# Optimization experiments

Measured on AMD Instinct MI355X. Metric: run time of the kernel, lower is better.

The kernel has to match this reference:

```python
import jax, jax.numpy as jnp
import numpy as np

E, FX, FE, H, OUT = 1_000_000, 32, 32, 64, 32
LN_EPS = 1e-5


def _ln(x, g, b):
    # LayerNorm over the channel (last) dim, elementwise_affine=True
    m = jnp.mean(x, axis=-1, keepdims=True)
    v = jnp.mean((x - m) ** 2, axis=-1, keepdims=True)
    return (x - m) * jax.lax.rsqrt(v + LN_EPS) * g + b


def setup_inputs() -> dict:
    key = jax.random.key(0)
    ks = jax.random.split(key, 6)
    d0 = 2 * FX + FE  # 96, the concat(src, dest, edge_attr) width
    src = jax.random.normal(ks[0], (E, FX), jnp.float32)
    dest = jax.random.normal(ks[1], (E, FX), jnp.float32)
    edge_attr = jax.random.normal(ks[2], (E, FE), jnp.float32)
    W1 = jax.random.normal(ks[3], (d0, H), jnp.float32) / np.float32(np.sqrt(d0))
    b1 = jnp.zeros((H,), jnp.float32)
    g1 = jnp.ones((H,), jnp.float32)
    be1 = jnp.zeros((H,), jnp.float32)
    W2 = jax.random.normal(ks[4], (H + d0, H), jnp.float32) / np.float32(np.sqrt(H + d0))
    b2 = jnp.zeros((H,), jnp.float32)
    g2 = jnp.ones((H,), jnp.float32)
    be2 = jnp.zeros((H,), jnp.float32)
    W3 = jax.random.normal(ks[5], (H, OUT), jnp.float32) / np.float32(np.sqrt(H))
    b3 = jnp.zeros((OUT,), jnp.float32)
    eb = jnp.zeros((E,), jnp.int32)  # edge-batch ids; unused (no GraphNorm in setup)
    return {"src": src, "dest": dest, "edge_attr": edge_attr,
            "W1": W1, "b1": b1, "g1": g1, "be1": be1,
            "W2": W2, "b2": b2, "g2": g2, "be2": be2,
            "W3": W3, "b3": b3, "eb": eb}


def reference(src, dest, edge_attr, W1, b1, g1, be1, W2, b2, g2, be2, W3, b3, eb):
    # out[0] = cat([src, dest, edge_attr], 1)
    x0 = jnp.concatenate([src, dest, edge_attr], axis=1)            # [E, 96]
    h = _ln(jax.nn.relu(x0 @ W1 + b1), g1, be1)                      # layers 0-2 -> [E, 64]
    # layer 3: shelf [3, 0] -> cat(out[3], out[0])
    h = _ln(jax.nn.relu(jnp.concatenate([h, x0], axis=1) @ W2 + b2), g2, be2)  # layers 3-5
    return h @ W3 + b3                                               # layer 6 -> [E, 32]
```

## Files before the change

### kernel.cpp

```cpp
#include <hip/hip_runtime.h>

typedef __bf16 bf16x8 __attribute__((ext_vector_type(8)));
typedef __bf16 bf16x4 __attribute__((ext_vector_type(4)));
typedef float  f32x4  __attribute__((ext_vector_type(4)));

#define NW 8
#define HPAD 68
#define NFRAG 36
#define LDS_WAIT() asm volatile("s_waitcnt lgkmcnt(0)" ::: "memory")

static __device__ __forceinline__ bf16x8 ld_frag_lds8(const __bf16* p) {
    bf16x4 lo = *(const bf16x4*)p;
    bf16x4 hi = *(const bf16x4*)(p + 4);
    bf16x8 r;
    r[0] = lo[0]; r[1] = lo[1]; r[2] = lo[2]; r[3] = lo[3];
    r[4] = hi[0]; r[5] = hi[1]; r[6] = hi[2]; r[7] = hi[3];
    return r;
}

static __device__ __forceinline__ bf16x8 cvt_frag(float4 v0, float4 v1) {
    bf16x8 r;
    r[0] = (__bf16)v0.x; r[1] = (__bf16)v0.y; r[2] = (__bf16)v0.z; r[3] = (__bf16)v0.w;
    r[4] = (__bf16)v1.x; r[5] = (__bf16)v1.y; r[6] = (__bf16)v1.z; r[7] = (__bf16)v1.w;
    return r;
}

static __device__ __forceinline__ void ln_epilogue(const f32x4* acc, const float* bv,
                                                   const float* gv, const float* ev,
                                                   __bf16* hp, int n16, int q) {
    float u[4][4];
    float sm[4] = {0.f, 0.f, 0.f, 0.f};
    float sq[4] = {0.f, 0.f, 0.f, 0.f};
#pragma unroll
    for (int t = 0; t < 4; ++t)
#pragma unroll
        for (int j = 0; j < 4; ++j) {
            float x = acc[t][j] + bv[t];
            x = fmaxf(x, 0.0f);
            u[t][j] = x;
            sm[j] += x;
            sq[j] += x * x;
        }
#pragma unroll
    for (int msk = 1; msk <= 8; msk <<= 1)
#pragma unroll
        for (int j = 0; j < 4; ++j) {
            sm[j] += __shfl_xor(sm[j], msk, 64);
            sq[j] += __shfl_xor(sq[j], msk, 64);
        }
    float mean[4], rstd[4];
#pragma unroll
    for (int j = 0; j < 4; ++j) {
        mean[j] = sm[j] * 0.015625f;
        float v = sq[j] * 0.015625f - mean[j] * mean[j];
        rstd[j] = rsqrtf(fmaxf(v, 0.0f) + 1e-5f);
    }
#pragma unroll
    for (int t = 0; t < 4; ++t)
#pragma unroll
        for (int j = 0; j < 4; ++j) {
            float y = (u[t][j] - mean[j]) * rstd[j] * gv[t] + ev[t];
            hp[(q * 4 + j) * HPAD + t * 16 + n16] = (__bf16)y;
        }
}

__global__ __launch_bounds__(512, 4)
void edge_model_kernel(const float* __restrict__ srcp,
                       const float* __restrict__ dstp,
                       const float* __restrict__ eap,
                       const float* __restrict__ W1, const float* __restrict__ b1,
                       const float* __restrict__ g1, const float* __restrict__ be1,
                       const float* __restrict__ W2, const float* __restrict__ b2,
                       const float* __restrict__ g2, const float* __restrict__ be2,
                       const float* __restrict__ W3, const float* __restrict__ b3,
                       float* __restrict__ out, int E) {
    __shared__ alignas(16) __bf16 wlds[NFRAG * 64 * 8];
    __shared__ alignas(16) __bf16 hs[NW][2][16 * HPAD];

    const int tid = threadIdx.x;
    const int w   = tid >> 6;
    const int l   = tid & 63;
    const int n16 = l & 15;
    const int q   = l >> 4;

    for (int idx = tid; idx < NFRAG * 64; idx += blockDim.x) {
        int fid = idx >> 6, fl = idx & 63;
        int lq = fl >> 4, ln = fl & 15;
        const float* Wsrc; int ldw, row0, col;
        if (fid < 12)      { int s = fid >> 2,        t = fid & 3;        Wsrc = W1; ldw = 64; row0 = s * 32 + lq * 8; col = t * 16 + ln; }
        else if (fid < 32) { int f = fid - 12, s = f >> 2, t = f & 3;     Wsrc = W2; ldw = 64; row0 = s * 32 + lq * 8; col = t * 16 + ln; }
        else               { int f = fid - 32, s = f >> 1, t = f & 1;     Wsrc = W3; ldw = 32; row0 = s * 32 + lq * 8; col = t * 16 + ln; }
        __bf16* dst = wlds + idx * 8;
#pragma unroll
        for (int jj = 0; jj < 8; ++jj)
            dst[jj] = (__bf16)Wsrc[(row0 + jj) * ldw + col];
    }

    float b1v[4], g1v[4], e1v[4], b2v[4], g2v[4], e2v[4], b3v[2];
#pragma unroll
    for (int t = 0; t < 4; ++t) {
        int c = t * 16 + n16;
        b1v[t] = b1[c]; g1v[t] = g1[c]; e1v[t] = be1[c];
        b2v[t] = b2[c]; g2v[t] = g2[c]; e2v[t] = be2[c];
    }
    b3v[0] = b3[n16];
    b3v[1] = b3[16 + n16];

    __syncthreads();

    const int nTiles = (E + 15) >> 4;
    const int stride = gridDim.x * NW;
    __bf16* h1p = &hs[w][0][0];
    __bf16* h2p = &hs[w][1][0];
    const __bf16* wl = wlds + l * 8;

    int tile = blockIdx.x * NW + w;
    if (tile >= nTiles) return;

    bf16x8 a0[3];
    {
        const size_t abase = (size_t)min((tile << 4) + n16, E - 1) * 32 + q * 8;
        a0[0] = cvt_frag(((const float4*)(srcp + abase))[0], ((const float4*)(srcp + abase))[1]);
        a0[1] = cvt_frag(((const float4*)(dstp + abase))[0], ((const float4*)(dstp + abase))[1]);
        a0[2] = cvt_frag(((const float4*)(eap  + abase))[0], ((const float4*)(eap  + abase))[1]);
    }

    for (;;) {
        const int e0 = tile << 4;
        const int nt = tile + stride;

        const int pt = (nt < nTiles) ? nt : tile;
        const size_t pbase = (size_t)min((pt << 4) + n16, E - 1) * 32 + q * 8;
        float4 p0a = ((const float4*)(srcp + pbase))[0];
        float4 p0b = ((const float4*)(srcp + pbase))[1];
        float4 p1a = ((const float4*)(dstp + pbase))[0];
        float4 p1b = ((const float4*)(dstp + pbase))[1];
        float4 p2a = ((const float4*)(eap  + pbase))[0];
        float4 p2b = ((const float4*)(eap  + pbase))[1];

        f32x4 acc1[4] = {};
#pragma unroll
        for (int s = 0; s < 3; ++s)
#pragma unroll
            for (int t = 0; t < 4; ++t) {
                bf16x8 wf = *(const bf16x8*)(wl + (s * 4 + t) * 512);
                acc1[t] = __builtin_amdgcn_mfma_f32_16x16x32_bf16(a0[s], wf, acc1[t], 0, 0, 0);
            }

        ln_epilogue(acc1, b1v, g1v, e1v, h1p, n16, q);
        LDS_WAIT();

        f32x4 acc2[4] = {};
        bf16x8 h1f0 = ld_frag_lds8(h1p + n16 * HPAD + q * 8);
        bf16x8 h1f1 = ld_frag_lds8(h1p + n16 * HPAD + 32 + q * 8);
#pragma unroll
        for (int t = 0; t < 4; ++t) {
            bf16x8 wf = *(const bf16x8*)(wl + (12 + t) * 512);
            acc2[t] = __builtin_amdgcn_mfma_f32_16x16x32_bf16(h1f0, wf, acc2[t], 0, 0, 0);
        }
#pragma unroll
        for (int t = 0; t < 4; ++t) {
            bf16x8 wf = *(const bf16x8*)(wl + (16 + t) * 512);
            acc2[t] = __builtin_amdgcn_mfma_f32_16x16x32_bf16(h1f1, wf, acc2[t], 0, 0, 0);
        }
#pragma unroll
        for (int s = 0; s < 3; ++s)
#pragma unroll
            for (int t = 0; t < 4; ++t) {
                bf16x8 wf = *(const bf16x8*)(wl + (20 + s * 4 + t) * 512);
                acc2[t] = __builtin_amdgcn_mfma_f32_16x16x32_bf16(a0[s], wf, acc2[t], 0, 0, 0);
            }

        ln_epilogue(acc2, b2v, g2v, e2v, h2p, n16, q);
        LDS_WAIT();

        f32x4 acc3[2] = {};
#pragma unroll
        for (int s = 0; s < 2; ++s) {
            bf16x8 h2f = ld_frag_lds8(h2p + n16 * HPAD + s * 32 + q * 8);
#pragma unroll
            for (int t = 0; t < 2; ++t) {
                bf16x8 wf = *(const bf16x8*)(wl + (32 + s * 2 + t) * 512);
                acc3[t] = __builtin_amdgcn_mfma_f32_16x16x32_bf16(h2f, wf, acc3[t], 0, 0, 0);
            }
        }

#pragma unroll
        for (int t = 0; t < 2; ++t)
#pragma unroll
            for (int j = 0; j < 4; ++j) {
                int r = e0 + q * 4 + j;
                if (r < E) out[(size_t)r * 32 + t * 16 + n16] = acc3[t][j] + b3v[t];
            }

        if (nt >= nTiles) break;
        tile = nt;
        a0[0] = cvt_frag(p0a, p0b);
        a0[1] = cvt_frag(p1a, p1b);
        a0[2] = cvt_frag(p2a, p2b);
    }
}

extern "C" void kernel_launch(void* const* d_in, const int* in_sizes, int n_in,
                              void* d_out, int out_size, void* d_ws, size_t ws_size,
                              hipStream_t stream) {
    (void)n_in; (void)out_size; (void)d_ws; (void)ws_size;
    const float* srcp = (const float*)d_in[0];
    const float* dstp = (const float*)d_in[1];
    const float* eap  = (const float*)d_in[2];
    const float* W1   = (const float*)d_in[3];
    const float* b1   = (const float*)d_in[4];
    const float* g1   = (const float*)d_in[5];
    const float* be1  = (const float*)d_in[6];
    const float* W2   = (const float*)d_in[7];
    const float* b2   = (const float*)d_in[8];
    const float* g2   = (const float*)d_in[9];
    const float* be2  = (const float*)d_in[10];
    const float* W3   = (const float*)d_in[11];
    const float* b3   = (const float*)d_in[12];
    float* out = (float*)d_out;

    const int E = in_sizes[0] / 32;
    const int nTiles = (E + 15) / 16;
    int blocks = (nTiles + NW - 1) / NW;
    if (blocks > 512) blocks = 512;

    edge_model_kernel<<<blocks, 512, 0, stream>>>(srcp, dstp, eap, W1, b1, g1, be1,
                                                  W2, b2, g2, be2, W3, b3, out, E);
}
```

Measured before the change: 414.5 us.

## Process two 16-edge tiles per wave to reuse weight fragments

Each wave now handles a 32-edge super-tile as two independent 16-row MFMA streams that share every weight fragment loaded from LDS. This halves LDS weight reads per edge and interleaves two independent MFMA chains to hide latency. The prefetch of the next super-tile's inputs is moved later, after the second LayerNorm, so fewer registers are live during the first two layers. The cost is doubled accumulator and input-fragment registers, which may spill under launch_bounds(512,4), and fewer waves in flight per edge.

```diff
diff --git a/kernel.cpp b/kernel.cpp
--- a/kernel.cpp
+++ b/kernel.cpp
@@ -108,80 +108,95 @@
 
     __syncthreads();
 
-    const int nTiles = (E + 15) >> 4;
+    const int nSuper = (E + 31) >> 5;
     const int stride = gridDim.x * NW;
-    __bf16* h1p = &hs[w][0][0];
-    __bf16* h2p = &hs[w][1][0];
+    __bf16* hA = &hs[w][0][0];
+    __bf16* hB = &hs[w][1][0];
     const __bf16* wl = wlds + l * 8;
 
-    int tile = blockIdx.x * NW + w;
-    if (tile >= nTiles) return;
-
-    bf16x8 a0[3];
+    int st = blockIdx.x * NW + w;
+    if (st >= nSuper) return;
+
+    bf16x8 a0A[3], a0B[3];
     {
-        const size_t abase = (size_t)min((tile << 4) + n16, E - 1) * 32 + q * 8;
-        a0[0] = cvt_frag(((const float4*)(srcp + abase))[0], ((const float4*)(srcp + abase))[1]);
-        a0[1] = cvt_frag(((const float4*)(dstp + abase))[0], ((const float4*)(dstp + abase))[1]);
-        a0[2] = cvt_frag(((const float4*)(eap  + abase))[0], ((const float4*)(eap  + abase))[1]);
+        const size_t baA = (size_t)min((st << 5) + n16,      E - 1) * 32 + q * 8;
+        const size_t baB = (size_t)min((st << 5) + 16 + n16, E - 1) * 32 + q * 8;
+        a0A[0] = cvt_frag(((const float4*)(srcp + baA))[0], ((const float4*)(srcp + baA))[1]);
+        a0A[1] = cvt_frag(((const float4*)(dstp + baA))[0], ((const float4*)(dstp + baA))[1]);
+        a0A[2] = cvt_frag(((const float4*)(eap  + baA))[0], ((const float4*)(eap  + baA))[1]);
+        a0B[0] = cvt_frag(((const float4*)(srcp + baB))[0], ((const float4*)(srcp + baB))[1]);
+        a0B[1] = cvt_frag(((const float4*)(dstp + baB))[0], ((const float4*)(dstp + baB))[1]);
+        a0B[2] = cvt_frag(((const float4*)(eap  + baB))[0], ((const float4*)(eap  + baB))[1]);
     }
 
     for (;;) {
-        const int e0 = tile << 4;
-        const int nt = tile + stride;
-
-        const int pt = (nt < nTiles) ? nt : tile;
-        const size_t pbase = (size_t)min((pt << 4) + n16, E - 1) * 32 + q * 8;
-        float4 p0a = ((const float4*)(srcp + pbase))[0];
-        float4 p0b = ((const float4*)(srcp + pbase))[1];
-        float4 p1a = ((const float4*)(dstp + pbase))[0];
-        float4 p1b = ((const float4*)(dstp + pbase))[1];
-        float4 p2a = ((const float4*)(eap  + pbase))[0];
-        float4 p2b = ((const float4*)(eap  + pbase))[1];
-
-        f32x4 acc1[4] = {};
+        const int e0 = st << 5;
+        const int ns = st + stride;
+
+        f32x4 accA1[4] = {}, accB1[4] = {};
 #pragma unroll
         for (int s = 0; s < 3; ++s)
 #pragma unroll
             for (int t = 0; t < 4; ++t) {
                 bf16x8 wf = *(const bf16x8*)(wl + (s * 4 + t) * 512);
-                acc1[t] = __builtin_amdgcn_mfma_f32_16x16x32_bf16(a0[s], wf, acc1[t], 0, 0, 0);
-            }
-
-        ln_epilogue(acc1, b1v, g1v, e1v, h1p, n16, q);
+                accA1[t] = __builtin_amdgcn_mfma_f32_16x16x32_bf16(a0A[s], wf, accA1[t], 0, 0, 0);
+                accB1[t] = __builtin_amdgcn_mfma_f32_16x16x32_bf16(a0B[s], wf, accB1[t], 0, 0, 0);
+            }
+
+        ln_epilogue(accA1, b1v, g1v, e1v, hA, n16, q);
+        ln_epilogue(accB1, b1v, g1v, e1v, hB, n16, q);
         LDS_WAIT();
 
-        f32x4 acc2[4] = {};
-        bf16x8 h1f0 = ld_frag_lds8(h1p + n16 * HPAD + q * 8);
-        bf16x8 h1f1 = ld_frag_lds8(h1p + n16 * HPAD + 32 + q * 8);
+        f32x4 accA2[4] = {}, accB2[4] = {};
+        bf16x8 hA0 = ld_frag_lds8(hA + n16 * HPAD + q * 8);
+        bf16x8 hA1 = ld_frag_lds8(hA + n16 * HPAD + 32 + q * 8);
+        bf16x8 hB0 = ld_frag_lds8(hB + n16 * HPAD + q * 8);
+        bf16x8 hB1 = ld_frag_lds8(hB + n16 * HPAD + 32 + q * 8);
 #pragma unroll
         for (int t = 0; t < 4; ++t) {
             bf16x8 wf = *(const bf16x8*)(wl + (12 + t) * 512);
-            acc2[t] = __builtin_amdgcn_mfma_f32_16x16x32_bf16(h1f0, wf, acc2[t], 0, 0, 0);
+            accA2[t] = __builtin_amdgcn_mfma_f32_16x16x32_bf16(hA0, wf, accA2[t], 0, 0, 0);
+            accB2[t] = __builtin_amdgcn_mfma_f32_16x16x32_bf16(hB0, wf, accB2[t], 0, 0, 0);
         }
 #pragma unroll
         for (int t = 0; t < 4; ++t) {
             bf16x8 wf = *(const bf16x8*)(wl + (16 + t) * 512);
-            acc2[t] = __builtin_amdgcn_mfma_f32_16x16x32_bf16(h1f1, wf, acc2[t], 0, 0, 0);
+            accA2[t] = __builtin_amdgcn_mfma_f32_16x16x32_bf16(hA1, wf, accA2[t], 0, 0, 0);
+            accB2[t] = __builtin_amdgcn_mfma_f32_16x16x32_bf16(hB1, wf, accB2[t], 0, 0, 0);
         }
 #pragma unroll
         for (int s = 0; s < 3; ++s)
 #pragma unroll
             for (int t = 0; t < 4; ++t) {
                 bf16x8 wf = *(const bf16x8*)(wl + (20 + s * 4 + t) * 512);
-                acc2[t] = __builtin_amdgcn_mfma_f32_16x16x32_bf16(a0[s], wf, acc2[t], 0, 0, 0);
-            }
-
-        ln_epilogue(acc2, b2v, g2v, e2v, h2p, n16, q);
+                accA2[t] = __builtin_amdgcn_mfma_f32_16x16x32_bf16(a0A[s], wf, accA2[t], 0, 0, 0);
+                accB2[t] = __builtin_amdgcn_mfma_f32_16x16x32_bf16(a0B[s], wf, accB2[t], 0, 0, 0);
+            }
+
+        ln_epilogue(accA2, b2v, g2v, e2v, hA, n16, q);
+        ln_epilogue(accB2, b2v, g2v, e2v, hB, n16, q);
         LDS_WAIT();
 
-        f32x4 acc3[2] = {};
+        const int pt = (ns < nSuper) ? ns : st;
+        const size_t pbA = (size_t)min((pt << 5) + n16,      E - 1) * 32 + q * 8;
+        const size_t pbB = (size_t)min((pt << 5) + 16 + n16, E - 1) * 32 + q * 8;
+        float4 pA0a = ((const float4*)(srcp + pbA))[0], pA0b = ((const float4*)(srcp + pbA))[1];
+        float4 pA1a = ((const float4*)(dstp + pbA))[0], pA1b = ((const float4*)(dstp + pbA))[1];
+        float4 pA2a = ((const float4*)(eap  + pbA))[0], pA2b = ((const float4*)(eap  + pbA))[1];
+        float4 pB0a = ((const float4*)(srcp + pbB))[0], pB0b = ((const float4*)(srcp + pbB))[1];
+        float4 pB1a = ((const float4*)(dstp + pbB))[0], pB1b = ((const float4*)(dstp + pbB))[1];
+        float4 pB2a = ((const float4*)(eap  + pbB))[0], pB2b = ((const float4*)(eap  + pbB))[1];
+
+        f32x4 accA3[2] = {}, accB3[2] = {};
 #pragma unroll
         for (int s = 0; s < 2; ++s) {
-            bf16x8 h2f = ld_frag_lds8(h2p + n16 * HPAD + s * 32 + q * 8);
+            bf16x8 hfA = ld_frag_lds8(hA + n16 * HPAD + s * 32 + q * 8);
+            bf16x8 hfB = ld_frag_lds8(hB + n16 * HPAD + s * 32 + q * 8);
 #pragma unroll
             for (int t = 0; t < 2; ++t) {
                 bf16x8 wf = *(const bf16x8*)(wl + (32 + s * 2 + t) * 512);
-                acc3[t] = __builtin_amdgcn_mfma_f32_16x16x32_bf16(h2f, wf, acc3[t], 0, 0, 0);
+                accA3[t] = __builtin_amdgcn_mfma_f32_16x16x32_bf16(hfA, wf, accA3[t], 0, 0, 0);
+                accB3[t] = __builtin_amdgcn_mfma_f32_16x16x32_bf16(hfB, wf, accB3[t], 0, 0, 0);
             }
         }
 
@@ -189,15 +204,20 @@
         for (int t = 0; t < 2; ++t)
 #pragma unroll
             for (int j = 0; j < 4; ++j) {
-                int r = e0 + q * 4 + j;
-                if (r < E) out[(size_t)r * 32 + t * 16 + n16] = acc3[t][j] + b3v[t];
-            }
-
-        if (nt >= nTiles) break;
-        tile = nt;
-        a0[0] = cvt_frag(p0a, p0b);
-        a0[1] = cvt_frag(p1a, p1b);
-        a0[2] = cvt_frag(p2a, p2b);
+                int rA = e0 + q * 4 + j;
+                int rB = e0 + 16 + q * 4 + j;
+                if (rA < E) out[(size_t)rA * 32 + t * 16 + n16] = accA3[t][j] + b3v[t];
+                if (rB < E) out[(size_t)rB * 32 + t * 16 + n16] = accB3[t][j] + b3v[t];
+            }
+
+        if (ns >= nSuper) break;
+        st = ns;
+        a0A[0] = cvt_frag(pA0a, pA0b);
+        a0A[1] = cvt_frag(pA1a, pA1b);
+        a0A[2] = cvt_frag(pA2a, pA2b);
+        a0B[0] = cvt_frag(pB0a, pB0b);
+        a0B[1] = cvt_frag(pB1a, pB1b);
+        a0B[2] = cvt_frag(pB2a, pB2b);
     }
 }
 
@@ -221,8 +241,8 @@
     float* out = (float*)d_out;
 
     const int E = in_sizes[0] / 32;
-    const int nTiles = (E + 15) / 16;
-    int blocks = (nTiles + NW - 1) / NW;
+    const int nSuper = (E + 31) / 32;
+    int blocks = (nSuper + NW - 1) / NW;
     if (blocks > 512) blocks = 512;
 
     edge_model_kernel<<<blocks, 512, 0, stream>>>(srcp, dstp, eap, W1, b1, g1, be1,
```

New measurement: 456.4 us. 10.1% more time.
